# Performance work log

Hardware: AMD Instinct MI355X
Metric: run time of the kernel (lower is better)

Reference implementation:

```python
import jax, jax.numpy as jnp
import numpy as np

B, S, D, H = 4, 2048, 1024, 16
DH = D // H


def setup_inputs() -> dict:
    key = jax.random.key(0)
    ks = jax.random.split(key, 11)
    s = 1.0 / np.sqrt(D)
    return {
        "query": jax.random.normal(ks[0], (B, S, D), jnp.float32),
        "key": jax.random.normal(ks[1], (B, S, D), jnp.float32),
        "value": jax.random.normal(ks[2], (B, S, D), jnp.float32),
        "Wq": jax.random.normal(ks[3], (D, D), jnp.float32) * s,
        "bq": jnp.zeros((D,), jnp.float32),
        "Wk": jax.random.normal(ks[4], (D, D), jnp.float32) * s,
        "bk": jnp.zeros((D,), jnp.float32),
        "Wv": jax.random.normal(ks[5], (D, D), jnp.float32) * s,
        "bv": jnp.zeros((D,), jnp.float32),
        "Wo": jax.random.normal(ks[6], (D, D), jnp.float32) * s,
        "bo": jnp.zeros((D,), jnp.float32),
    }


def reference(query, key, value, Wq, bq, Wk, bk, Wv, bv, Wo, bo):
    # QKV projections (nn.Linear: x @ W.T + b; here W stored as [in, out])
    q = (query @ Wq + bq).reshape(B, S, H, DH).transpose(0, 2, 1, 3)  # [B,H,S,DH]
    k = (key @ Wk + bk).reshape(B, S, H, DH).transpose(0, 2, 1, 3)
    v = (value @ Wv + bv).reshape(B, S, H, DH).transpose(0, 2, 1, 3)
    # scaled dot-product attention (dropout in eval mode -> identity)
    scores = jnp.einsum("bhqd,bhkd->bhqk", q, k) / jnp.sqrt(jnp.float32(DH))
    attn = jax.nn.softmax(scores, axis=-1)
    out = jnp.einsum("bhqk,bhkd->bhqd", attn, v)  # [B,H,S,DH]
    out = out.transpose(0, 2, 1, 3).reshape(B, S, D)
    return out @ Wo + bo
```

## Files before the change

kernel.cpp:

```cpp
#include <hip/hip_runtime.h>


typedef __bf16 bf16x8 __attribute__((ext_vector_type(8)));
typedef __bf16 bf16x4 __attribute__((ext_vector_type(4)));
typedef float f32x4 __attribute__((ext_vector_type(4)));

#define GLAS __attribute__((address_space(1)))
#define LDSAS __attribute__((address_space(3)))

__device__ __forceinline__ void gl16(const void* g, void* l) {
  __builtin_amdgcn_global_load_lds((GLAS void*)const_cast<void*>(g),
                                   (LDSAS void*)l, 16, 0, 0);
}

__global__ __launch_bounds__(256) void wt_cvt(const float* __restrict__ w,
                                              __bf16* __restrict__ wt, float scl) {
  __shared__ float t[32][33];
  const int n0 = blockIdx.x * 32, k0 = blockIdx.y * 32;
  const int x = threadIdx.x, y = threadIdx.y;
#pragma unroll
  for (int i = 0; i < 32; i += 8) t[y + i][x] = w[(k0 + y + i) * 1024 + n0 + x];
  __syncthreads();
#pragma unroll
  for (int i = 0; i < 32; i += 8)
    wt[(n0 + y + i) * 1024 + (k0 + x)] = (__bf16)(t[x][y + i] * scl);
}

__global__ __launch_bounds__(256) void cvt_k(const float* __restrict__ in,
                                             __bf16* __restrict__ out) {
  const int i = (blockIdx.x * 256 + threadIdx.x) * 8;
  const float4 f0 = *(const float4*)(in + i);
  const float4 f1 = *(const float4*)(in + i + 4);
  bf16x8 o;
  o[0] = (__bf16)f0.x; o[1] = (__bf16)f0.y; o[2] = (__bf16)f0.z; o[3] = (__bf16)f0.w;
  o[4] = (__bf16)f1.x; o[5] = (__bf16)f1.y; o[6] = (__bf16)f1.z; o[7] = (__bf16)f1.w;
  *(bf16x8*)(out + i) = o;
}

__global__ __launch_bounds__(256) void gemm_qkv(
    const __bf16* __restrict__ Abase, const __bf16* __restrict__ Wbase,
    const float* __restrict__ bq, const float* __restrict__ bk,
    const float* __restrict__ bv, float sclq,
    __bf16* __restrict__ Qp, __bf16* __restrict__ Kp, __bf16* __restrict__ Vtp) {
  __shared__ __align__(16) char smem[32768];
  const int tid = threadIdx.x, wid = tid >> 6, lane = tid & 63;
  const int wr = wid >> 1, wc = wid & 1;
  const int fid = blockIdx.x + (blockIdx.y << 3);
  const int nid = (fid & 7) * 192 + (fid >> 3);
  const int bx = nid & 7, by = nid >> 3;
  const int sel = by >> 6;
  const int m0 = (by & 63) * 128, n0 = bx * 128;
  const int lr = lane & 15, lg = lane >> 4;

  const int srow = lane >> 3;
  const int scl8 = (lane & 7) ^ srow;
  const __bf16* A  = Abase + sel * 8388608;
  const __bf16* BT = Wbase + sel * 1048576;
  const __bf16* Ab = A + (m0 + wid * 32 + srow) * 1024 + scl8 * 8;
  const __bf16* Bb = BT + (n0 + wid * 32 + srow) * 1024 + scl8 * 8;
  char* AsW = smem + wid * 4096;
  char* BsW = smem + 16384 + wid * 4096;

  f32x4 acc[4][4] = {};

  for (int k0 = 0; k0 < 1024; k0 += 64) {
#pragma unroll
    for (int i = 0; i < 4; ++i) {
      gl16(Ab + i * 8192 + k0, AsW + i * 1024);
      gl16(Bb + i * 8192 + k0, BsW + i * 1024);
    }
    __syncthreads();
#pragma unroll
    for (int ks = 0; ks < 2; ++ks) {
      bf16x8 af[4], bfv[4];
      const int co = (ks * 64 + lg * 16) ^ ((lr & 7) << 4);
#pragma unroll
      for (int i = 0; i < 4; ++i) {
        af[i]  = *(const bf16x8*)(smem + (wr * 64 + i * 16 + lr) * 128 + co);
        bfv[i] = *(const bf16x8*)(smem + 16384 + (wc * 64 + i * 16 + lr) * 128 + co);
      }
#pragma unroll
      for (int i = 0; i < 4; ++i)
#pragma unroll
        for (int j = 0; j < 4; ++j)
          acc[i][j] = __builtin_amdgcn_mfma_f32_16x16x32_bf16(af[i], bfv[j], acc[i][j], 0, 0, 0);
    }
    __syncthreads();
  }

  const float* bias = sel == 0 ? bq : (sel == 1 ? bk : bv);
  const float bsc = sel == 0 ? sclq : 1.f;
  __bf16* outp = sel == 0 ? Qp : (sel == 1 ? Kp : Vtp);
#pragma unroll
  for (int i = 0; i < 4; ++i)
#pragma unroll
    for (int j = 0; j < 4; ++j) {
      const int n = n0 + wc * 64 + j * 16 + lr;
      const float bb = bias[n] * bsc;
#pragma unroll
      for (int r = 0; r < 4; ++r) {
        const int m = m0 + wr * 64 + i * 16 + lg * 4 + r;
        const float v = acc[i][j][r] + bb;
        const int b = m >> 11, s = m & 2047;
        const int h = n >> 6, dh = n & 63;
        if (sel < 2)
          outp[(((b * 16 + h) * 2048 + s) << 6) + dh] = (__bf16)v;
        else
          outp[(((b * 16 + h) * 64 + dh) << 11) + s] = (__bf16)v;
      }
    }
}

__global__ __launch_bounds__(256) void gemm_o(const __bf16* __restrict__ A,
                                              const __bf16* __restrict__ BT,
                                              const float* __restrict__ bias,
                                              float* __restrict__ outp) {
  __shared__ __align__(16) char smem[32768];
  const int tid = threadIdx.x, wid = tid >> 6, lane = tid & 63;
  const int wr = wid >> 1, wc = wid & 1;
  const int fid = blockIdx.x + (blockIdx.y << 3);
  const int nid = (fid & 7) * 64 + (fid >> 3);
  const int m0 = (nid >> 3) * 128, n0 = (nid & 7) * 128;
  const int lr = lane & 15, lg = lane >> 4;

  const int srow = lane >> 3;
  const int scl8 = (lane & 7) ^ srow;
  const __bf16* Ab = A + (m0 + wid * 32 + srow) * 1024 + scl8 * 8;
  const __bf16* Bb = BT + (n0 + wid * 32 + srow) * 1024 + scl8 * 8;
  char* AsW = smem + wid * 4096;
  char* BsW = smem + 16384 + wid * 4096;

  f32x4 acc[4][4] = {};

  for (int k0 = 0; k0 < 1024; k0 += 64) {
#pragma unroll
    for (int i = 0; i < 4; ++i) {
      gl16(Ab + i * 8192 + k0, AsW + i * 1024);
      gl16(Bb + i * 8192 + k0, BsW + i * 1024);
    }
    __syncthreads();
#pragma unroll
    for (int ks = 0; ks < 2; ++ks) {
      bf16x8 af[4], bfv[4];
      const int co = (ks * 64 + lg * 16) ^ ((lr & 7) << 4);
#pragma unroll
      for (int i = 0; i < 4; ++i) {
        af[i]  = *(const bf16x8*)(smem + (wr * 64 + i * 16 + lr) * 128 + co);
        bfv[i] = *(const bf16x8*)(smem + 16384 + (wc * 64 + i * 16 + lr) * 128 + co);
      }
#pragma unroll
      for (int i = 0; i < 4; ++i)
#pragma unroll
        for (int j = 0; j < 4; ++j)
          acc[i][j] = __builtin_amdgcn_mfma_f32_16x16x32_bf16(af[i], bfv[j], acc[i][j], 0, 0, 0);
    }
    __syncthreads();
  }

#pragma unroll
  for (int i = 0; i < 4; ++i)
#pragma unroll
    for (int j = 0; j < 4; ++j) {
      const int n = n0 + wc * 64 + j * 16 + lr;
      const float bb = bias[n];
#pragma unroll
      for (int r = 0; r < 4; ++r) {
        const int m = m0 + wr * 64 + i * 16 + lg * 4 + r;
        outp[m * 1024 + n] = acc[i][j][r] + bb;
      }
    }
}

__global__ __launch_bounds__(256) void attn_k(const __bf16* __restrict__ Qp,
                                              const __bf16* __restrict__ Kp,
                                              const __bf16* __restrict__ Vt,
                                              __bf16* __restrict__ ctx) {
  __shared__ __align__(16) char smem[40960];
  const int tid = threadIdx.x, wid = tid >> 6, lane = tid & 63;
  const int lr = lane & 15, lg = lane >> 4;
  const int fid = blockIdx.x + (blockIdx.y << 4);
  const int nid = (fid & 7) * 128 + (fid >> 3);
  const int bh = nid >> 4;
  const int q0 = (nid & 15) * 128 + wid * 32;
  const int S = 2048;

  const int srow = lane >> 3;
  const int scl8 = (lane & 7) ^ srow;
  const __bf16* Kbase = Kp + (bh * S + srow) * 64 + scl8 * 8;
  const __bf16* Vbase = Vt + (bh * 64 + srow) * S + scl8 * 8;
  char* Ps = smem + 32768 + wid * 2048;

  bf16x8 aq[2][2];
#pragma unroll
  for (int qs = 0; qs < 2; ++qs)
#pragma unroll
    for (int ks = 0; ks < 2; ++ks)
      aq[qs][ks] = *(const bf16x8*)(Qp + (bh * S + q0 + qs * 16 + lr) * 64 +
                                    ks * 32 + lg * 8);

  float m_run[2] = {-1e30f, -1e30f}, l_run[2] = {0.f, 0.f};
  f32x4 acc_o[2][4] = {};

#pragma unroll
  for (int i = 0; i < 2; ++i) {
    const int ch = wid * 2 + i;
    gl16(Kbase + ch * 512, smem + ch * 1024);
    gl16(Vbase + ch * 16384, smem + 16384 + ch * 1024);
  }

  int cur = 0;
  for (int t = 0; t < 32; ++t) {
    __syncthreads();
    if (t + 1 < 32) {
      const int kv1 = (t + 1) * 64;
      char* Kd = smem + (cur ^ 1) * 8192;
      char* Vd = smem + 16384 + (cur ^ 1) * 8192;
#pragma unroll
      for (int i = 0; i < 2; ++i) {
        const int ch = wid * 2 + i;
        gl16(Kbase + kv1 * 64 + ch * 512, Kd + ch * 1024);
        gl16(Vbase + kv1 + ch * 16384, Vd + ch * 1024);
      }
    }
    const char* Ks = smem + cur * 8192;
    const char* Vs = smem + 16384 + cur * 8192;

    f32x4 sc[2][4] = {};
    __builtin_amdgcn_s_setprio(1);
#pragma unroll
    for (int cb = 0; cb < 4; ++cb) {
#pragma unroll
      for (int ks = 0; ks < 2; ++ks) {
        const int krow = cb * 16 + lr;
        const bf16x8 kf = *(const bf16x8*)(Ks + krow * 128 +
                                           ((ks * 64 + lg * 16) ^ ((krow & 7) << 4)));
        sc[0][cb] = __builtin_amdgcn_mfma_f32_16x16x32_bf16(kf, aq[0][ks], sc[0][cb], 0, 0, 0);
        sc[1][cb] = __builtin_amdgcn_mfma_f32_16x16x32_bf16(kf, aq[1][ks], sc[1][cb], 0, 0, 0);
      }
    }
    __builtin_amdgcn_s_setprio(0);

    bf16x8 pa[2][2];
#pragma unroll
    for (int qs = 0; qs < 2; ++qs) {
      float mx = sc[qs][0][0];
#pragma unroll
      for (int cb = 0; cb < 4; ++cb)
#pragma unroll
        for (int r = 0; r < 4; ++r) mx = fmaxf(mx, sc[qs][cb][r]);
      mx = fmaxf(mx, __shfl_xor(mx, 16, 64));
      mx = fmaxf(mx, __shfl_xor(mx, 32, 64));
      if (!__all(mx <= m_run[qs] + 8.f)) {
        const float mnew = fmaxf(m_run[qs], mx);
        const float corr = __builtin_amdgcn_exp2f(m_run[qs] - mnew);
        m_run[qs] = mnew;
        l_run[qs] *= corr;
        float corrv[4];
#pragma unroll
        for (int r = 0; r < 4; ++r) corrv[r] = __shfl(corr, lg * 4 + r, 64);
#pragma unroll
        for (int dhb = 0; dhb < 4; ++dhb)
#pragma unroll
          for (int r = 0; r < 4; ++r) acc_o[qs][dhb][r] *= corrv[r];
      }
      float rs = 0.f;
#pragma unroll
      for (int cb = 0; cb < 4; ++cb) {
        bf16x4 pk;
#pragma unroll
        for (int r = 0; r < 4; ++r) {
          const float p = __builtin_amdgcn_exp2f(sc[qs][cb][r] - m_run[qs]);
          rs += p;
          pk[r] = (__bf16)p;
        }
        *(bf16x4*)(Ps + lr * 128 + ((cb * 32 + lg * 8) ^ ((lr & 7) << 4))) = pk;
      }
      rs += __shfl_xor(rs, 16, 64);
      rs += __shfl_xor(rs, 32, 64);
      l_run[qs] += rs;
#pragma unroll
      for (int ks = 0; ks < 2; ++ks)
        pa[qs][ks] = *(const bf16x8*)(Ps + lr * 128 +
                                      ((ks * 64 + lg * 16) ^ ((lr & 7) << 4)));
    }

    __builtin_amdgcn_s_setprio(1);
#pragma unroll
    for (int dhb = 0; dhb < 4; ++dhb) {
#pragma unroll
      for (int ks = 0; ks < 2; ++ks) {
        const int vrow = dhb * 16 + lr;
        const bf16x8 vf = *(const bf16x8*)(Vs + vrow * 128 +
                                           ((ks * 64 + lg * 16) ^ ((vrow & 7) << 4)));
        acc_o[0][dhb] = __builtin_amdgcn_mfma_f32_16x16x32_bf16(pa[0][ks], vf, acc_o[0][dhb], 0, 0, 0);
        acc_o[1][dhb] = __builtin_amdgcn_mfma_f32_16x16x32_bf16(pa[1][ks], vf, acc_o[1][dhb], 0, 0, 0);
      }
    }
    __builtin_amdgcn_s_setprio(0);
    cur ^= 1;
  }

  const int b = bh >> 4, h = bh & 15;
#pragma unroll
  for (int qs = 0; qs < 2; ++qs) {
    float linv[4];
#pragma unroll
    for (int r = 0; r < 4; ++r) linv[r] = 1.f / __shfl(l_run[qs], lg * 4 + r, 64);
#pragma unroll
    for (int dhb = 0; dhb < 4; ++dhb)
#pragma unroll
      for (int r = 0; r < 4; ++r) {
        const int sr = q0 + qs * 16 + lg * 4 + r;
        const int d = h * 64 + dhb * 16 + lr;
        ctx[(b * 2048 + sr) * 1024 + d] = (__bf16)(acc_o[qs][dhb][r] * linv[r]);
      }
  }
}

extern "C" void kernel_launch(void* const* d_in, const int* in_sizes, int n_in,
                              void* d_out, int out_size, void* d_ws, size_t ws_size,
                              hipStream_t stream) {
  const float* query = (const float*)d_in[0];
  const float* key   = (const float*)d_in[1];
  const float* value = (const float*)d_in[2];
  const float* Wq = (const float*)d_in[3];
  const float* bq = (const float*)d_in[4];
  const float* Wk = (const float*)d_in[5];
  const float* bk = (const float*)d_in[6];
  const float* Wv = (const float*)d_in[7];
  const float* bv = (const float*)d_in[8];
  const float* Wo = (const float*)d_in[9];
  const float* bo = (const float*)d_in[10];

  char* ws = (char*)d_ws;
  const size_t MiB = 1048576;
  __bf16* Wqkv = (__bf16*)(ws);
  __bf16* WoT  = (__bf16*)(ws + 6 * MiB);
  __bf16* Abf  = (__bf16*)(ws + 8 * MiB);
  __bf16* Qp   = (__bf16*)(ws + 56 * MiB);
  __bf16* Kp   = (__bf16*)(ws + 72 * MiB);
  __bf16* Vt   = (__bf16*)(ws + 88 * MiB);
  __bf16* ctx  = Abf;

  const float SCL = 0.125f * 1.44269504088896340736f;

  const dim3 tb(32, 8);
  wt_cvt<<<dim3(32, 32), tb, 0, stream>>>(Wq, Wqkv,              SCL);
  wt_cvt<<<dim3(32, 32), tb, 0, stream>>>(Wk, Wqkv + 1048576,    1.f);
  wt_cvt<<<dim3(32, 32), tb, 0, stream>>>(Wv, Wqkv + 2097152,    1.f);
  wt_cvt<<<dim3(32, 32), tb, 0, stream>>>(Wo, WoT,               1.f);

  cvt_k<<<4096, 256, 0, stream>>>(query, Abf);
  cvt_k<<<4096, 256, 0, stream>>>(key,   Abf + 8388608);
  cvt_k<<<4096, 256, 0, stream>>>(value, Abf + 16777216);

  gemm_qkv<<<dim3(8, 192), 256, 0, stream>>>(Abf, Wqkv, bq, bk, bv, SCL, Qp, Kp, Vt);

  attn_k<<<dim3(16, 64), 256, 0, stream>>>(Qp, Kp, Vt, ctx);

  gemm_o<<<dim3(8, 64), 256, 0, stream>>>(ctx, WoT, bo, (float*)d_out);
}
```

Baseline: 392.6 us.

## Double-buffer LDS in projection GEMMs and merge conversion kernel launches

Both projection GEMMs now use two LDS stages: the async global-to-LDS loads for the next K tile are issued before the current tile is computed, leaving one barrier per iteration, so memory latency is hidden behind MFMA work. The four weight-transpose launches and the three input-cast launches are each merged into a single launch that selects its source from the block index, which cuts launch overhead. Doubling LDS to 64KB per block may lower the number of resident blocks per CU.

After: 370.3 us. 5.7% less time.

```diff
diff --git a/kernel.cpp b/kernel.cpp
--- a/kernel.cpp
+++ b/kernel.cpp
@@ -13,10 +13,17 @@
                                    (LDSAS void*)l, 16, 0, 0);
 }
 
-__global__ __launch_bounds__(256) void wt_cvt(const float* __restrict__ w,
-                                              __bf16* __restrict__ wt, float scl) {
+__global__ __launch_bounds__(256) void wt_cvt4(const float* __restrict__ wq,
+                                               const float* __restrict__ wk,
+                                               const float* __restrict__ wv,
+                                               const float* __restrict__ wo,
+                                               __bf16* __restrict__ wt4, float sclq) {
   __shared__ float t[32][33];
-  const int n0 = blockIdx.x * 32, k0 = blockIdx.y * 32;
+  const int wsel = blockIdx.y >> 5;
+  const float* w = wsel == 0 ? wq : (wsel == 1 ? wk : (wsel == 2 ? wv : wo));
+  const float scl = wsel == 0 ? sclq : 1.f;
+  __bf16* wt = wt4 + wsel * 1048576;
+  const int n0 = blockIdx.x * 32, k0 = (blockIdx.y & 31) * 32;
   const int x = threadIdx.x, y = threadIdx.y;
 #pragma unroll
   for (int i = 0; i < 32; i += 8) t[y + i][x] = w[(k0 + y + i) * 1024 + n0 + x];
@@ -26,15 +33,19 @@
     wt[(n0 + y + i) * 1024 + (k0 + x)] = (__bf16)(t[x][y + i] * scl);
 }
 
-__global__ __launch_bounds__(256) void cvt_k(const float* __restrict__ in,
-                                             __bf16* __restrict__ out) {
-  const int i = (blockIdx.x * 256 + threadIdx.x) * 8;
+__global__ __launch_bounds__(256) void cvt_k3(const float* __restrict__ q,
+                                              const float* __restrict__ k,
+                                              const float* __restrict__ v,
+                                              __bf16* __restrict__ out) {
+  const int sel = blockIdx.x >> 12;
+  const float* in = sel == 0 ? q : (sel == 1 ? k : v);
+  const int i = ((blockIdx.x & 4095) * 256 + threadIdx.x) * 8;
   const float4 f0 = *(const float4*)(in + i);
   const float4 f1 = *(const float4*)(in + i + 4);
   bf16x8 o;
   o[0] = (__bf16)f0.x; o[1] = (__bf16)f0.y; o[2] = (__bf16)f0.z; o[3] = (__bf16)f0.w;
   o[4] = (__bf16)f1.x; o[5] = (__bf16)f1.y; o[6] = (__bf16)f1.z; o[7] = (__bf16)f1.w;
-  *(bf16x8*)(out + i) = o;
+  *(bf16x8*)(out + sel * 8388608 + i) = o;
 }
 
 __global__ __launch_bounds__(256) void gemm_qkv(
@@ -42,7 +53,7 @@
     const float* __restrict__ bq, const float* __restrict__ bk,
     const float* __restrict__ bv, float sclq,
     __bf16* __restrict__ Qp, __bf16* __restrict__ Kp, __bf16* __restrict__ Vtp) {
-  __shared__ __align__(16) char smem[32768];
+  __shared__ __align__(16) char smem[65536];
   const int tid = threadIdx.x, wid = tid >> 6, lane = tid & 63;
   const int wr = wid >> 1, wc = wid & 1;
   const int fid = blockIdx.x + (blockIdx.y << 3);
@@ -58,26 +69,37 @@
   const __bf16* BT = Wbase + sel * 1048576;
   const __bf16* Ab = A + (m0 + wid * 32 + srow) * 1024 + scl8 * 8;
   const __bf16* Bb = BT + (n0 + wid * 32 + srow) * 1024 + scl8 * 8;
-  char* AsW = smem + wid * 4096;
-  char* BsW = smem + 16384 + wid * 4096;
 
   f32x4 acc[4][4] = {};
 
+#pragma unroll
+  for (int i = 0; i < 4; ++i) {
+    gl16(Ab + i * 8192, smem + wid * 4096 + i * 1024);
+    gl16(Bb + i * 8192, smem + 32768 + wid * 4096 + i * 1024);
+  }
+
+  int cur = 0;
   for (int k0 = 0; k0 < 1024; k0 += 64) {
-#pragma unroll
-    for (int i = 0; i < 4; ++i) {
-      gl16(Ab + i * 8192 + k0, AsW + i * 1024);
-      gl16(Bb + i * 8192 + k0, BsW + i * 1024);
-    }
     __syncthreads();
+    if (k0 + 64 < 1024) {
+      char* Ad = smem + (cur ^ 1) * 16384 + wid * 4096;
+      char* Bd = smem + 32768 + (cur ^ 1) * 16384 + wid * 4096;
+#pragma unroll
+      for (int i = 0; i < 4; ++i) {
+        gl16(Ab + i * 8192 + k0 + 64, Ad + i * 1024);
+        gl16(Bb + i * 8192 + k0 + 64, Bd + i * 1024);
+      }
+    }
+    const char* As = smem + cur * 16384;
+    const char* Bs = smem + 32768 + cur * 16384;
 #pragma unroll
     for (int ks = 0; ks < 2; ++ks) {
       bf16x8 af[4], bfv[4];
       const int co = (ks * 64 + lg * 16) ^ ((lr & 7) << 4);
 #pragma unroll
       for (int i = 0; i < 4; ++i) {
-        af[i]  = *(const bf16x8*)(smem + (wr * 64 + i * 16 + lr) * 128 + co);
-        bfv[i] = *(const bf16x8*)(smem + 16384 + (wc * 64 + i * 16 + lr) * 128 + co);
+        af[i]  = *(const bf16x8*)(As + (wr * 64 + i * 16 + lr) * 128 + co);
+        bfv[i] = *(const bf16x8*)(Bs + (wc * 64 + i * 16 + lr) * 128 + co);
       }
 #pragma unroll
       for (int i = 0; i < 4; ++i)
@@ -85,7 +107,7 @@
         for (int j = 0; j < 4; ++j)
           acc[i][j] = __builtin_amdgcn_mfma_f32_16x16x32_bf16(af[i], bfv[j], acc[i][j], 0, 0, 0);
     }
-    __syncthreads();
+    cur ^= 1;
   }
 
   const float* bias = sel == 0 ? bq : (sel == 1 ? bk : bv);
@@ -115,7 +137,7 @@
                                               const __bf16* __restrict__ BT,
                                               const float* __restrict__ bias,
                                               float* __restrict__ outp) {
-  __shared__ __align__(16) char smem[32768];
+  __shared__ __align__(16) char smem[65536];
   const int tid = threadIdx.x, wid = tid >> 6, lane = tid & 63;
   const int wr = wid >> 1, wc = wid & 1;
   const int fid = blockIdx.x + (blockIdx.y << 3);
@@ -127,26 +149,37 @@
   const int scl8 = (lane & 7) ^ srow;
   const __bf16* Ab = A + (m0 + wid * 32 + srow) * 1024 + scl8 * 8;
   const __bf16* Bb = BT + (n0 + wid * 32 + srow) * 1024 + scl8 * 8;
-  char* AsW = smem + wid * 4096;
-  char* BsW = smem + 16384 + wid * 4096;
 
   f32x4 acc[4][4] = {};
 
+#pragma unroll
+  for (int i = 0; i < 4; ++i) {
+    gl16(Ab + i * 8192, smem + wid * 4096 + i * 1024);
+    gl16(Bb + i * 8192, smem + 32768 + wid * 4096 + i * 1024);
+  }
+
+  int cur = 0;
   for (int k0 = 0; k0 < 1024; k0 += 64) {
-#pragma unroll
-    for (int i = 0; i < 4; ++i) {
-      gl16(Ab + i * 8192 + k0, AsW + i * 1024);
-      gl16(Bb + i * 8192 + k0, BsW + i * 1024);
-    }
     __syncthreads();
+    if (k0 + 64 < 1024) {
+      char* Ad = smem + (cur ^ 1) * 16384 + wid * 4096;
+      char* Bd = smem + 32768 + (cur ^ 1) * 16384 + wid * 4096;
+#pragma unroll
+      for (int i = 0; i < 4; ++i) {
+        gl16(Ab + i * 8192 + k0 + 64, Ad + i * 1024);
+        gl16(Bb + i * 8192 + k0 + 64, Bd + i * 1024);
+      }
+    }
+    const char* As = smem + cur * 16384;
+    const char* Bs = smem + 32768 + cur * 16384;
 #pragma unroll
     for (int ks = 0; ks < 2; ++ks) {
       bf16x8 af[4], bfv[4];
       const int co = (ks * 64 + lg * 16) ^ ((lr & 7) << 4);
 #pragma unroll
       for (int i = 0; i < 4; ++i) {
-        af[i]  = *(const bf16x8*)(smem + (wr * 64 + i * 16 + lr) * 128 + co);
-        bfv[i] = *(const bf16x8*)(smem + 16384 + (wc * 64 + i * 16 + lr) * 128 + co);
+        af[i]  = *(const bf16x8*)(As + (wr * 64 + i * 16 + lr) * 128 + co);
+        bfv[i] = *(const bf16x8*)(Bs + (wc * 64 + i * 16 + lr) * 128 + co);
       }
 #pragma unroll
       for (int i = 0; i < 4; ++i)
@@ -154,7 +187,7 @@
         for (int j = 0; j < 4; ++j)
           acc[i][j] = __builtin_amdgcn_mfma_f32_16x16x32_bf16(af[i], bfv[j], acc[i][j], 0, 0, 0);
     }
-    __syncthreads();
+    cur ^= 1;
   }
 
 #pragma unroll
@@ -334,29 +367,21 @@
 
   char* ws = (char*)d_ws;
   const size_t MiB = 1048576;
-  __bf16* Wqkv = (__bf16*)(ws);
-  __bf16* WoT  = (__bf16*)(ws + 6 * MiB);
-  __bf16* Abf  = (__bf16*)(ws + 8 * MiB);
-  __bf16* Qp   = (__bf16*)(ws + 56 * MiB);
-  __bf16* Kp   = (__bf16*)(ws + 72 * MiB);
-  __bf16* Vt   = (__bf16*)(ws + 88 * MiB);
-  __bf16* ctx  = Abf;
+  __bf16* Wt4 = (__bf16*)(ws);
+  __bf16* Abf = (__bf16*)(ws + 8 * MiB);
+  __bf16* Qp  = (__bf16*)(ws + 56 * MiB);
+  __bf16* Kp  = (__bf16*)(ws + 72 * MiB);
+  __bf16* Vt  = (__bf16*)(ws + 88 * MiB);
+  __bf16* ctx = Abf;
 
   const float SCL = 0.125f * 1.44269504088896340736f;
 
-  const dim3 tb(32, 8);
-  wt_cvt<<<dim3(32, 32), tb, 0, stream>>>(Wq, Wqkv,              SCL);
-  wt_cvt<<<dim3(32, 32), tb, 0, stream>>>(Wk, Wqkv + 1048576,    1.f);
-  wt_cvt<<<dim3(32, 32), tb, 0, stream>>>(Wv, Wqkv + 2097152,    1.f);
-  wt_cvt<<<dim3(32, 32), tb, 0, stream>>>(Wo, WoT,               1.f);
-
-  cvt_k<<<4096, 256, 0, stream>>>(query, Abf);
-  cvt_k<<<4096, 256, 0, stream>>>(key,   Abf + 8388608);
-  cvt_k<<<4096, 256, 0, stream>>>(value, Abf + 16777216);
-
-  gemm_qkv<<<dim3(8, 192), 256, 0, stream>>>(Abf, Wqkv, bq, bk, bv, SCL, Qp, Kp, Vt);
+  wt_cvt4<<<dim3(32, 128), dim3(32, 8), 0, stream>>>(Wq, Wk, Wv, Wo, Wt4, SCL);
+  cvt_k3<<<12288, 256, 0, stream>>>(query, key, value, Abf);
+
+  gemm_qkv<<<dim3(8, 192), 256, 0, stream>>>(Abf, Wt4, bq, bk, bv, SCL, Qp, Kp, Vt);
 
   attn_k<<<dim3(16, 64), 256, 0, stream>>>(Qp, Kp, Vt, ctx);
 
-  gemm_o<<<dim3(8, 64), 256, 0, stream>>>(ctx, WoT, bo, (float*)d_out);
-}
+  gemm_o<<<dim3(8, 64), 256, 0, stream>>>(ctx, Wt4 + 3145728, bo, (float*)d_out);
+}
```
